# Optimization experiments

Hardware: AMD Instinct MI355X
Metric: run time of the kernel (lower is better)

## Reference

```python
import jax, jax.numpy as jnp
import numpy as np

N_LAYER = 2
N_HEAD = 12
D = 768
B = 4
L = 1024
LN_EPS = 1e-6
NEG = jnp.float32(-1e9)


def setup_inputs() -> dict:
    key = jax.random.key(0)
    ks = jax.random.split(key, 12)
    s = 0.02
    wshp = (N_LAYER, 4, D, D)
    return {
        "h_a": jax.random.normal(ks[0], (B, L, D), jnp.float32),
        "h_b": jax.random.normal(ks[1], (B, L, D), jnp.float32),
        "adj_a": jax.random.randint(ks[2], (B, L, L), 0, 2, jnp.int32),
        "adj_b": jax.random.randint(ks[3], (B, L, L), 0, 2, jnp.int32),
        "adj_ab": jax.random.randint(ks[4], (B, L, L), 0, 2, jnp.int32),
        "adj_ba": jax.random.randint(ks[5], (B, L, L), 0, 2, jnp.int32),
        "Wq": jax.random.normal(ks[6], wshp, jnp.float32) * s,
        "Wk": jax.random.normal(ks[7], wshp, jnp.float32) * s,
        "Wv": jax.random.normal(ks[8], wshp, jnp.float32) * s,
        "Wf": jax.random.normal(ks[9], wshp, jnp.float32) * s,
        "ln_g": jnp.ones((N_LAYER, 4, D), jnp.float32),
        "ln_b": jnp.zeros((N_LAYER, 4, D), jnp.float32),
    }


def _mha(xq, xk, xv, mask, Wq, Wk, Wv, Wf, g, b):
    # xq: [B, Lq, D]; mask: [B, Lq, Lk] (0 = masked out)
    Bq, Lq, d = xq.shape
    dk = d // N_HEAD
    q = (xq @ Wq).reshape(Bq, Lq, N_HEAD, dk).transpose(0, 2, 1, 3)
    k = (xk @ Wk).reshape(Bq, -1, N_HEAD, dk).transpose(0, 2, 1, 3)
    v = (xv @ Wv).reshape(Bq, -1, N_HEAD, dk).transpose(0, 2, 1, 3)
    attn = jnp.einsum('bhqd,bhkd->bhqk', q, k) / jnp.sqrt(jnp.float32(dk))
    attn = jnp.where(mask[:, None, :, :] == 0, NEG, attn)
    attn = jax.nn.softmax(attn, axis=-1)
    o = jnp.einsum('bhqk,bhkd->bhqd', attn, v)
    o = o.transpose(0, 2, 1, 3).reshape(Bq, Lq, d)
    o = o @ Wf + xq  # residual (dropout is identity in eval)
    mu = jnp.mean(o, axis=-1, keepdims=True)
    var = jnp.var(o, axis=-1, keepdims=True)
    return (o - mu) * jax.lax.rsqrt(var + LN_EPS) * g + b


def reference(h_a, h_b, adj_a, adj_b, adj_ab, adj_ba, Wq, Wk, Wv, Wf, ln_g, ln_b):
    input_a, input_b = h_a, h_b
    for i in range(N_LAYER):
        a2a = _mha(h_a, h_a, h_a, adj_a, Wq[i, 0], Wk[i, 0], Wv[i, 0], Wf[i, 0], ln_g[i, 0], ln_b[i, 0])
        b2b = _mha(h_b, h_b, h_b, adj_b, Wq[i, 1], Wk[i, 1], Wv[i, 1], Wf[i, 1], ln_g[i, 1], ln_b[i, 1])
        a2b = _mha(h_b, h_a, h_a, adj_ab, Wq[i, 2], Wk[i, 2], Wv[i, 2], Wf[i, 2], ln_g[i, 2], ln_b[i, 2])
        b2a = _mha(h_a, h_b, h_b, adj_ba, Wq[i, 3], Wk[i, 3], Wv[i, 3], Wf[i, 3], ln_g[i, 3], ln_b[i, 3])
        h_a = jax.nn.relu(a2a + b2a)
        h_b = jax.nn.relu(b2b + a2b)
    return (input_a + h_a, input_b + h_b)
```

## Files before the change

### kernel.cpp

```cpp
#include <hip/hip_runtime.h>
#include <stdint.h>

#define NLAYER 2
#define NHEAD 12
#define D 768
#define BB 4
#define LL 1024
#define M (BB*LL)
#define DK 64

typedef unsigned short u16;
typedef unsigned int u32;
typedef unsigned long long u64;
typedef __attribute__((ext_vector_type(8))) __bf16 bf16x8;
typedef __attribute__((ext_vector_type(4))) float f32x4;

__device__ __forceinline__ u16 f2b(float f) {
  u32 u = __float_as_uint(f);
  u += 0x7fffu + ((u >> 16) & 1u);
  return (u16)(u >> 16);
}
__device__ __forceinline__ float b2f(u16 h) {
  return __uint_as_float(((u32)h) << 16);
}
__device__ __forceinline__ f32x4 mfma16(bf16x8 a, bf16x8 b, f32x4 c) {
  return __builtin_amdgcn_mfma_f32_16x16x32_bf16(a, b, c, 0, 0, 0);
}
__device__ __forceinline__ void gl_lds16(const u16* g, u16* l) {
  __builtin_amdgcn_global_load_lds((const __attribute__((address_space(1))) void*)(g),
                                   (__attribute__((address_space(3))) void*)(l), 16, 0, 0);
}

__global__ void cast_f32_bf16(const float* __restrict__ src, u16* __restrict__ dst, int n) {
  int i = (blockIdx.x * 256 + threadIdx.x) * 4;
  if (i + 3 < n) {
    float4 v = *(const float4*)(src + i);
    dst[i+0] = f2b(v.x); dst[i+1] = f2b(v.y); dst[i+2] = f2b(v.z); dst[i+3] = f2b(v.w);
  }
}

__global__ void wtrans(const float* __restrict__ Wq, const float* __restrict__ Wk,
                       const float* __restrict__ Wv, const float* __restrict__ Wf,
                       u16* __restrict__ wtr) {
  int z = blockIdx.z;
  int layer = z >> 4, mat = (z >> 2) & 3, s = z & 3;
  const float* src = (mat==0?Wq:mat==1?Wk:mat==2?Wv:Wf) + (size_t)(layer*4 + s)*D*D;
  u16* dst = wtr + (size_t)z*D*D;
  __shared__ float tile[32][33];
  int x0 = blockIdx.x*32, y0 = blockIdx.y*32;
  int tx = threadIdx.x & 31, ty = threadIdx.x >> 5;
  #pragma unroll
  for (int i=0;i<4;++i) tile[ty + i*8][tx] = src[(size_t)(y0 + ty + i*8)*D + x0 + tx];
  __syncthreads();
  #pragma unroll
  for (int i=0;i<4;++i) dst[(size_t)(x0 + ty + i*8)*D + y0 + tx] = f2b(tile[tx][ty + i*8]);
}

__global__ __launch_bounds__(256) void pack_adj(const int* __restrict__ a0, const int* __restrict__ a1,
                                                const int* __restrict__ a2, const int* __restrict__ a3,
                                                u64* __restrict__ mb) {
  const int s = blockIdx.y;
  const int* __restrict__ src = s==0?a0:s==1?a1:s==2?a2:a3;
  u64* dst = mb + (size_t)s * (BB*LL*LL/64);
  const int lane = threadIdx.x & 63;
  const int w0 = blockIdx.x*4 + (threadIdx.x>>6);
  const int wstep = gridDim.x*4;
  for (int w = w0; w < BB*LL*LL/64; w += wstep) {
    int v = src[(size_t)w*64 + lane];
    u64 m = __ballot(v != 0);
    if (lane == 0) dst[w] = m;
  }
}

__device__ __forceinline__ void gemm128(const u16* __restrict__ A, const u16* __restrict__ W,
                                        u16* __restrict__ C, int vtrans) {
  __shared__ __align__(16) u16 As[128*32];
  __shared__ __align__(16) u16 Bs[128*32];
  const int t = threadIdx.x;
  const int wave = t >> 6, lane = t & 63, lg = lane >> 4, lr = lane & 15;
  const int wr = wave >> 1, wc = wave & 1;
  const int m0 = blockIdx.x * 128, n0 = blockIdx.y * 128;
  f32x4 acc[4][4] = {};
  const int srow = wave*32 + (lane >> 2);
  const int scol = (lane & 3) << 3;
  const u16* ga0 = A + (size_t)(m0 + srow)*D + scol;
  const u16* gb0 = W + (size_t)(n0 + srow)*D + scol;
  u16* lA0 = &As[(wave*32)*32];
  u16* lA1 = &As[(wave*32 + 16)*32];
  u16* lB0 = &Bs[(wave*32)*32];
  u16* lB1 = &Bs[(wave*32 + 16)*32];
  for (int kk = 0; kk < D; kk += 32) {
    __syncthreads();
    gl_lds16(ga0 + kk,          lA0);
    gl_lds16(ga0 + kk + 16*D,   lA1);
    gl_lds16(gb0 + kk,          lB0);
    gl_lds16(gb0 + kk + 16*D,   lB1);
    __syncthreads();
    bf16x8 af[4], bfr[4];
    #pragma unroll
    for (int mi=0;mi<4;++mi) af[mi] = *(const bf16x8*)(&As[(wr*64 + mi*16 + lr)*32 + lg*8]);
    #pragma unroll
    for (int ni=0;ni<4;++ni) bfr[ni] = *(const bf16x8*)(&Bs[(wc*64 + ni*16 + lr)*32 + lg*8]);
    #pragma unroll
    for (int mi=0;mi<4;++mi)
      #pragma unroll
      for (int ni=0;ni<4;++ni)
        acc[mi][ni] = mfma16(af[mi], bfr[ni], acc[mi][ni]);
  }
  if (!vtrans) {
    #pragma unroll
    for (int mi=0;mi<4;++mi)
      #pragma unroll
      for (int ni=0;ni<4;++ni) {
        int col = n0 + wc*64 + ni*16 + lr;
        #pragma unroll
        for (int r=0;r<4;++r) {
          int row = m0 + wr*64 + mi*16 + lg*4 + r;
          C[(size_t)row*D + col] = f2b(acc[mi][ni][r]);
        }
      }
  } else {
    #pragma unroll
    for (int mi=0;mi<4;++mi)
      #pragma unroll
      for (int ni=0;ni<4;++ni) {
        int col = n0 + wc*64 + ni*16 + lr;
        int h = col >> 6, d = col & 63;
        #pragma unroll
        for (int r=0;r<4;++r) {
          int row = m0 + wr*64 + mi*16 + lg*4 + r;
          int p = ((r >> 1) << 5) | (lg << 3) | (mi << 1) | (r & 1);
          int lperm = (row & ~63) | p;
          int b = row >> 10, l = lperm & 1023;
          C[(((size_t)((b*NHEAD + h)<<6) + d) << 10) + l] = f2b(acc[mi][ni][r]);
        }
      }
  }
}

__global__ __launch_bounds__(256) void qkv_gemm(const u16* __restrict__ hA, const u16* __restrict__ hB,
                        const u16* __restrict__ wtr,
                        u16* __restrict__ Qb, u16* __restrict__ Kb, u16* __restrict__ Vtb, int layer) {
  int z = blockIdx.z;
  int s = z / 3, which = z % 3;
  const u16* X;
  if (which == 0) X = (s==0||s==3) ? hA : hB;
  else            X = (s==0||s==2) ? hA : hB;
  const u16* W = wtr + (size_t)((layer*4 + which)*4 + s)*D*D;
  u16* Cb = (which==0 ? Qb : which==1 ? Kb : Vtb) + (size_t)s*M*D;
  gemm128(X, W, Cb, which == 2 ? 1 : 0);
}

__global__ __launch_bounds__(256) void oproj_gemm(const u16* __restrict__ Ob, const u16* __restrict__ wtr,
                          u16* __restrict__ OPb, int layer) {
  int s = blockIdx.z;
  const u16* W = wtr + (size_t)((layer*4 + 3)*4 + s)*D*D;
  gemm128(Ob + (size_t)s*M*D, W, OPb + (size_t)s*M*D, 0);
}

#define CSC 0.1803368801111204f

__global__ __launch_bounds__(512) void attn_kernel(const u16* __restrict__ Qb, const u16* __restrict__ Kb,
                           const u16* __restrict__ Vtb,
                           const u64* __restrict__ mbits,
                           u16* __restrict__ Ob) {
  int bid = blockIdx.x + 8*(blockIdx.y + 48*blockIdx.z);
  int logical = (bid & 7)*192 + (bid >> 3);
  const int qt = logical & 7;
  const int bhs = logical >> 3;
  const int s = bhs / 48;
  const int bh = bhs % 48;
  const int b = bh / NHEAD, h = bh % NHEAD;

  const int t = threadIdx.x, wave = t >> 6, lane = t & 63, lg = lane >> 4, lr = lane & 15;
  const u16* Q = Qb + (size_t)s*M*D;
  const u16* K = Kb + (size_t)s*M*D;
  u16* O = Ob + (size_t)s*M*D;
  const u64* mbs = mbits + (size_t)s*(BB*LL*LL/64) + (size_t)b*(LL*LL/64);

  __shared__ __align__(16) u16 Ks[64][72];
  __shared__ __align__(16) u16 Vts[64][72];

  const int q0 = qt*128 + wave*16;
  bf16x8 qf0 = *(const bf16x8*)(Q + (size_t)(b*LL + q0 + lr)*D + h*DK + lg*8);
  bf16x8 qf1 = *(const bf16x8*)(Q + (size_t)(b*LL + q0 + lr)*D + h*DK + 32 + lg*8);

  f32x4 of[4] = {};
  float lrow = 0.f;

  const int kr = t >> 3, kc = (t & 7) << 3;
  const u16* Kp  = K + (size_t)(b*LL + kr)*D + h*DK + kc;
  const u16* Vtp = Vtb + (size_t)s*M*D + ((size_t)(bh*64 + kr) << 10) + kc;

  uint4 ka = *(const uint4*)(Kp);
  uint4 va = *(const uint4*)(Vtp);
  const int mstride = LL/64;
  u64 mw = mbs[(size_t)(q0 + lr)*mstride];
  u64 mwn;

  for (int kt = 0; kt < LL; kt += 64) {
    __syncthreads();
    *(uint4*)(&Ks[kr][kc])  = ka;
    *(uint4*)(&Vts[kr][kc]) = va;
    if (kt + 64 < LL) {
      ka = *(const uint4*)(Kp + (size_t)(kt+64)*D);
      va = *(const uint4*)(Vtp + kt + 64);
      mwn = mbs[(size_t)(q0 + lr)*mstride + (kt >> 6) + 1];
    }
    __syncthreads();

    f32x4 sfr[4];
    __builtin_amdgcn_s_setprio(1);
    #pragma unroll
    for (int c=0;c<4;++c) {
      bf16x8 kf0 = *(const bf16x8*)(&Ks[c*16+lr][lg*8]);
      bf16x8 kf1 = *(const bf16x8*)(&Ks[c*16+lr][32 + lg*8]);
      f32x4 z = {0.f,0.f,0.f,0.f};
      z = mfma16(kf0, qf0, z);
      z = mfma16(kf1, qf1, z);
      sfr[c] = z;
    }
    __builtin_amdgcn_s_setprio(0);

    u32 wlo = (u32)(mw >> (lg*4));
    u32 whi = (u32)(mw >> (lg*4 + 32));
    float pw[4][4];
    #pragma unroll
    for (int c=0;c<4;++c) {
      u32 wsel = (c < 2) ? wlo : whi;
      int sh = (c & 1) << 4;
      #pragma unroll
      for (int r=0;r<4;++r) {
        float e = __builtin_amdgcn_exp2f(sfr[c][r]*CSC);
        e = ((wsel >> (sh + r)) & 1u) ? e : 0.f;
        pw[c][r] = e;
        lrow += e;
      }
    }
    mw = mwn;

    union { u32 u[4]; bf16x8 v; } a0, a1;
    #pragma unroll
    for (int c=0;c<4;++c) {
      a0.u[c] = (__float_as_uint(pw[c][0]) >> 16) | (__float_as_uint(pw[c][1]) & 0xffff0000u);
      a1.u[c] = (__float_as_uint(pw[c][2]) >> 16) | (__float_as_uint(pw[c][3]) & 0xffff0000u);
    }

    __builtin_amdgcn_s_setprio(1);
    #pragma unroll
    for (int ni=0;ni<4;++ni) {
      bf16x8 vf0 = *(const bf16x8*)(&Vts[ni*16+lr][lg*8]);
      bf16x8 vf1 = *(const bf16x8*)(&Vts[ni*16+lr][32 + lg*8]);
      of[ni] = mfma16(a0.v, vf0, of[ni]);
      of[ni] = mfma16(a1.v, vf1, of[ni]);
    }
    __builtin_amdgcn_s_setprio(0);
  }

  lrow += __shfl_xor(lrow, 16, 64);
  lrow += __shfl_xor(lrow, 32, 64);

  #pragma unroll
  for (int r=0;r<4;++r) {
    float l = __shfl(lrow, lg*4 + r, 64);
    float inv = 1.0f / fmaxf(l, 1e-35f);
    int row = b*LL + q0 + lg*4 + r;
    #pragma unroll
    for (int ni=0;ni<4;++ni)
      O[(size_t)row*D + h*DK + ni*16 + lr] = f2b(of[ni][r] * inv);
  }
}

__global__ __launch_bounds__(256) void epilogue(const u16* __restrict__ OPb,
                        u16* __restrict__ hA, u16* __restrict__ hB,
                        const float* __restrict__ lng, const float* __restrict__ lnb,
                        const float* __restrict__ inA, const float* __restrict__ inB,
                        float* __restrict__ outA, float* __restrict__ outB,
                        int layer, int last) {
  const int row = blockIdx.x;
  const int t = threadIdx.x;
  __shared__ float red[8];
  float lnv[4][3];
  #pragma unroll
  for (int s=0;s<4;++s) {
    const u16* xq = (s==0||s==3) ? hA : hB;
    float o[3]; float sum=0.f, sq=0.f;
    #pragma unroll
    for (int j=0;j<3;++j) {
      int c = t + j*256;
      float v = b2f(OPb[((size_t)s*M + row)*D + c]) + b2f(xq[(size_t)row*D + c]);
      o[j]=v; sum+=v; sq += v*v;
    }
    #pragma unroll
    for (int off=32; off>0; off>>=1) { sum += __shfl_down(sum, off, 64); sq += __shfl_down(sq, off, 64); }
    int wv = t>>6, ln = t&63;
    if (ln==0) { red[wv] = sum; red[4+wv] = sq; }
    __syncthreads();
    sum = red[0]+red[1]+red[2]+red[3];
    sq  = red[4]+red[5]+red[6]+red[7];
    __syncthreads();
    float mu = sum * (1.0f/D);
    float var = sq * (1.0f/D) - mu*mu;
    float rstd = rsqrtf(var + 1e-6f);
    #pragma unroll
    for (int j=0;j<3;++j) {
      int c = t + j*256;
      lnv[s][j] = (o[j]-mu)*rstd * lng[(layer*4+s)*D + c] + lnb[(layer*4+s)*D + c];
    }
  }
  #pragma unroll
  for (int j=0;j<3;++j) {
    int c = t + j*256;
    float ha = fmaxf(lnv[0][j]+lnv[3][j], 0.f);
    float hb = fmaxf(lnv[1][j]+lnv[2][j], 0.f);
    hA[(size_t)row*D + c] = f2b(ha);
    hB[(size_t)row*D + c] = f2b(hb);
    if (last) {
      outA[(size_t)row*D + c] = inA[(size_t)row*D + c] + ha;
      outB[(size_t)row*D + c] = inB[(size_t)row*D + c] + hb;
    }
  }
}

extern "C" void kernel_launch(void* const* d_in, const int* in_sizes, int n_in,
                              void* d_out, int out_size, void* d_ws, size_t ws_size,
                              hipStream_t stream) {
  const float* h_a = (const float*)d_in[0];
  const float* h_b = (const float*)d_in[1];
  const int* adjA  = (const int*)d_in[2];
  const int* adjB  = (const int*)d_in[3];
  const int* adjAB = (const int*)d_in[4];
  const int* adjBA = (const int*)d_in[5];
  const float* Wq  = (const float*)d_in[6];
  const float* Wk  = (const float*)d_in[7];
  const float* Wv  = (const float*)d_in[8];
  const float* Wf  = (const float*)d_in[9];
  const float* lng = (const float*)d_in[10];
  const float* lnb = (const float*)d_in[11];
  float* outA = (float*)d_out;
  float* outB = outA + (size_t)M*D;

  char* ws = (char*)d_ws;
  size_t off = 0;
  auto alloc = [&](size_t bytes) { void* p = ws + off; off += (bytes + 255) & ~(size_t)255; return p; };
  u16* wtr = (u16*)alloc((size_t)32*D*D*2);
  u16* hAb = (u16*)alloc((size_t)M*D*2);
  u16* hBb = (u16*)alloc((size_t)M*D*2);
  u16* Qb  = (u16*)alloc((size_t)4*M*D*2);
  u16* Kb  = (u16*)alloc((size_t)4*M*D*2);
  u16* Vtb = (u16*)alloc((size_t)4*M*D*2);
  u16* Ob  = (u16*)alloc((size_t)4*M*D*2);
  u64* mbits = (u64*)alloc((size_t)4*BB*LL*LL/64*8);
  u16* OPb = Qb;

  int n = M*D;
  cast_f32_bf16<<<dim3(n/4/256), 256, 0, stream>>>(h_a, hAb, n);
  cast_f32_bf16<<<dim3(n/4/256), 256, 0, stream>>>(h_b, hBb, n);
  wtrans<<<dim3(24,24,32), 256, 0, stream>>>(Wq, Wk, Wv, Wf, wtr);
  pack_adj<<<dim3(2048,4), 256, 0, stream>>>(adjA, adjB, adjAB, adjBA, mbits);

  for (int layer = 0; layer < NLAYER; ++layer) {
    qkv_gemm<<<dim3(32,6,12), 256, 0, stream>>>(hAb, hBb, wtr, Qb, Kb, Vtb, layer);
    attn_kernel<<<dim3(8,48,4), 512, 0, stream>>>(Qb, Kb, Vtb, mbits, Ob);
    oproj_gemm<<<dim3(32,6,4), 256, 0, stream>>>(Ob, wtr, OPb, layer);
    epilogue<<<dim3(M), 256, 0, stream>>>(OPb, hAb, hBb, lng, lnb, h_a, h_b, outA, outB,
                                          layer, layer == NLAYER-1 ? 1 : 0);
  }
}
```

Baseline: 483.3 us.

## Double-buffer GEMM LDS tiles and remap blocks across XCDs

The shared GEMM helper now keeps two LDS buffers and prefetches the next K-slice while the current one feeds the MFMAs. It waits only on the older loads with explicit vmcnt waits and raises wave priority around the MFMA block. The QKV and output-projection kernels remap linear block IDs so consecutive logical tiles of the same matrix land on the same XCD, which should improve L2 reuse. The cost is twice the LDS per block and hand-written waitcnt logic, which must match the instruction count of gl_lds16.

```diff
diff --git a/kernel.cpp b/kernel.cpp
--- a/kernel.cpp
+++ b/kernel.cpp
@@ -73,40 +73,54 @@
 }
 
 __device__ __forceinline__ void gemm128(const u16* __restrict__ A, const u16* __restrict__ W,
-                                        u16* __restrict__ C, int vtrans) {
-  __shared__ __align__(16) u16 As[128*32];
-  __shared__ __align__(16) u16 Bs[128*32];
+                                        u16* __restrict__ C, int vtrans,
+                                        int m0, int n0) {
+  __shared__ __align__(16) u16 As[2][128*32];
+  __shared__ __align__(16) u16 Bs[2][128*32];
   const int t = threadIdx.x;
   const int wave = t >> 6, lane = t & 63, lg = lane >> 4, lr = lane & 15;
   const int wr = wave >> 1, wc = wave & 1;
-  const int m0 = blockIdx.x * 128, n0 = blockIdx.y * 128;
   f32x4 acc[4][4] = {};
   const int srow = wave*32 + (lane >> 2);
   const int scol = (lane & 3) << 3;
   const u16* ga0 = A + (size_t)(m0 + srow)*D + scol;
   const u16* gb0 = W + (size_t)(n0 + srow)*D + scol;
-  u16* lA0 = &As[(wave*32)*32];
-  u16* lA1 = &As[(wave*32 + 16)*32];
-  u16* lB0 = &Bs[(wave*32)*32];
-  u16* lB1 = &Bs[(wave*32 + 16)*32];
-  for (int kk = 0; kk < D; kk += 32) {
-    __syncthreads();
-    gl_lds16(ga0 + kk,          lA0);
-    gl_lds16(ga0 + kk + 16*D,   lA1);
-    gl_lds16(gb0 + kk,          lB0);
-    gl_lds16(gb0 + kk + 16*D,   lB1);
-    __syncthreads();
+  const int l0 = (wave*32)*32, l1 = (wave*32 + 16)*32;
+
+  gl_lds16(ga0,        &As[0][l0]);
+  gl_lds16(ga0 + 16*D, &As[0][l1]);
+  gl_lds16(gb0,        &Bs[0][l0]);
+  gl_lds16(gb0 + 16*D, &Bs[0][l1]);
+
+  #pragma unroll 2
+  for (int tt = 0; tt < 24; ++tt) {
+    const int cur = tt & 1;
+    __builtin_amdgcn_s_barrier();
+    if (tt < 23) {
+      const int kk = tt*32 + 32;
+      gl_lds16(ga0 + kk,        &As[cur^1][l0]);
+      gl_lds16(ga0 + kk + 16*D, &As[cur^1][l1]);
+      gl_lds16(gb0 + kk,        &Bs[cur^1][l0]);
+      gl_lds16(gb0 + kk + 16*D, &Bs[cur^1][l1]);
+      asm volatile("s_waitcnt vmcnt(4)" ::: "memory");
+    } else {
+      asm volatile("s_waitcnt vmcnt(0)" ::: "memory");
+    }
+    __builtin_amdgcn_s_barrier();
     bf16x8 af[4], bfr[4];
     #pragma unroll
-    for (int mi=0;mi<4;++mi) af[mi] = *(const bf16x8*)(&As[(wr*64 + mi*16 + lr)*32 + lg*8]);
-    #pragma unroll
-    for (int ni=0;ni<4;++ni) bfr[ni] = *(const bf16x8*)(&Bs[(wc*64 + ni*16 + lr)*32 + lg*8]);
+    for (int mi=0;mi<4;++mi) af[mi] = *(const bf16x8*)(&As[cur][(wr*64 + mi*16 + lr)*32 + lg*8]);
+    #pragma unroll
+    for (int ni=0;ni<4;++ni) bfr[ni] = *(const bf16x8*)(&Bs[cur][(wc*64 + ni*16 + lr)*32 + lg*8]);
+    __builtin_amdgcn_s_setprio(1);
     #pragma unroll
     for (int mi=0;mi<4;++mi)
       #pragma unroll
       for (int ni=0;ni<4;++ni)
         acc[mi][ni] = mfma16(af[mi], bfr[ni], acc[mi][ni]);
-  }
+    __builtin_amdgcn_s_setprio(0);
+  }
+
   if (!vtrans) {
     #pragma unroll
     for (int mi=0;mi<4;++mi)
@@ -141,21 +155,27 @@
 __global__ __launch_bounds__(256) void qkv_gemm(const u16* __restrict__ hA, const u16* __restrict__ hB,
                         const u16* __restrict__ wtr,
                         u16* __restrict__ Qb, u16* __restrict__ Kb, u16* __restrict__ Vtb, int layer) {
-  int z = blockIdx.z;
+  int bid = blockIdx.x + 32*(blockIdx.y + 6*blockIdx.z);
+  int logical = (bid & 7)*288 + (bid >> 3);
+  int z = logical / 192, rem = logical % 192;
+  int x = rem / 6, y = rem % 6;
   int s = z / 3, which = z % 3;
   const u16* X;
   if (which == 0) X = (s==0||s==3) ? hA : hB;
   else            X = (s==0||s==2) ? hA : hB;
   const u16* W = wtr + (size_t)((layer*4 + which)*4 + s)*D*D;
   u16* Cb = (which==0 ? Qb : which==1 ? Kb : Vtb) + (size_t)s*M*D;
-  gemm128(X, W, Cb, which == 2 ? 1 : 0);
+  gemm128(X, W, Cb, which == 2 ? 1 : 0, x*128, y*128);
 }
 
 __global__ __launch_bounds__(256) void oproj_gemm(const u16* __restrict__ Ob, const u16* __restrict__ wtr,
                           u16* __restrict__ OPb, int layer) {
-  int s = blockIdx.z;
+  int bid = blockIdx.x + 32*(blockIdx.y + 6*blockIdx.z);
+  int logical = (bid & 7)*96 + (bid >> 3);
+  int s = logical / 192, rem = logical % 192;
+  int x = rem / 6, y = rem % 6;
   const u16* W = wtr + (size_t)((layer*4 + 3)*4 + s)*D*D;
-  gemm128(Ob + (size_t)s*M*D, W, OPb + (size_t)s*M*D, 0);
+  gemm128(Ob + (size_t)s*M*D, W, OPb + (size_t)s*M*D, 0, x*128, y*128);
 }
 
 #define CSC 0.1803368801111204f
```

After: 527.0 us. 1.09x slower.
